# Optimization experiments

Measured on AMD Instinct MI355X. Metric: run time of the kernel, lower is better.

Reference implementation:

```python
import jax, jax.numpy as jnp
import numpy as np

L1, L2, L3 = 3072, 15, 32
NUM_PSQT = 8
NUM_LS = 8
NUM_FEATURES = 22528
B = 1024
MAX_ACTIVE = 32


def setup_inputs() -> dict:
    key = jax.random.key(0)
    ks = jax.random.split(key, 12)
    inp = {
        "us": jax.random.uniform(ks[0], (B, 1), dtype=jnp.float32),
        "them": jax.random.uniform(ks[1], (B, 1), dtype=jnp.float32),
        "white_indices": jax.random.randint(ks[2], (B, MAX_ACTIVE), 0, NUM_FEATURES, dtype=jnp.int64 if jax.config.jax_enable_x64 else jnp.int32),
        "white_values": jnp.ones((B, MAX_ACTIVE), dtype=jnp.float32),
        "black_indices": jax.random.randint(ks[3], (B, MAX_ACTIVE), 0, NUM_FEATURES, dtype=jnp.int64 if jax.config.jax_enable_x64 else jnp.int32),
        "black_values": jnp.ones((B, MAX_ACTIVE), dtype=jnp.float32),
        "psqt_indices": jax.random.randint(ks[4], (B,), 0, NUM_PSQT),
        "layer_stack_indices": jax.random.randint(ks[5], (B,), 0, NUM_LS),
        # feature transformer (sparse embedding) params: width L1 + NUM_PSQT
        "ft_weight": jax.random.normal(ks[6], (NUM_FEATURES, L1 + NUM_PSQT), dtype=jnp.float32) * 0.01,
        "ft_bias": jax.random.normal(ks[7], (L1 + NUM_PSQT,), dtype=jnp.float32) * 0.01,
        # bucketed layer stacks: l1 outputs L2 + 1 (extra unit is the skip connection)
        "W1": jax.random.normal(ks[8], (NUM_LS, L2 + 1, L1), dtype=jnp.float32) * 0.02,
        "b1": jnp.zeros((NUM_LS, L2 + 1), dtype=jnp.float32),
        "W2": jax.random.normal(ks[9], (NUM_LS, L3, 2 * L2), dtype=jnp.float32) * 0.1,
        "b2": jnp.zeros((NUM_LS, L3), dtype=jnp.float32),
        "W3": jax.random.normal(ks[10], (NUM_LS, 1, L3), dtype=jnp.float32) * 0.1,
        "b3": jnp.zeros((NUM_LS, 1), dtype=jnp.float32),
    }
    return inp


def _ft_accumulate(ft_weight, ft_bias, indices, values):
    # sparse feature accumulator: sum of gathered rows weighted by values
    rows = ft_weight[indices]                    # [B, F, L1+NUM_PSQT]
    return jnp.einsum("bfd,bf->bd", rows, values) + ft_bias


def _select_bucket(x_all, bucket_idx):
    # x_all: [B, K, D] -> [B, D] selecting per-sample bucket
    return jnp.take_along_axis(x_all, bucket_idx[:, None, None], axis=1)[:, 0]


def reference(us, them, white_indices, white_values, black_indices, black_values,
              psqt_indices, layer_stack_indices,
              ft_weight, ft_bias, W1, b1, W2, b2, W3, b3):
    wp = _ft_accumulate(ft_weight, ft_bias, white_indices, white_values)
    bp = _ft_accumulate(ft_weight, ft_bias, black_indices, black_values)
    w, wpsqt = wp[:, :L1], wp[:, L1:]
    b, bpsqt = bp[:, :L1], bp[:, L1:]

    # perspective mix + clamp + pairwise squared activation
    l0 = us * jnp.concatenate([w, b], axis=1) + them * jnp.concatenate([b, w], axis=1)
    l0 = jnp.clip(l0, 0.0, 1.0)                  # [B, 2*L1]
    h = L1 // 2
    l0 = jnp.concatenate([l0[:, :h] * l0[:, h:2 * h],
                          l0[:, 2 * h:3 * h] * l0[:, 3 * h:]], axis=1) * (127.0 / 128.0)  # [B, L1]

    # bucketed layer stacks (compute all buckets, tiny dims, then select)
    li = layer_stack_indices
    l1c = _select_bucket(jnp.einsum("bi,koi->bko", l0, W1) + b1, li)   # [B, L2+1]
    l1x, l1y = l1c[:, :L2], l1c[:, L2:]
    l1x = jnp.clip(jnp.concatenate([l1x * l1x, l1x], axis=1), 0.0, 1.0)  # [B, 2*L2]
    l2c = _select_bucket(jnp.einsum("bi,koi->bko", l1x, W2) + b2, li)  # [B, L3]
    l2x = jnp.clip(l2c, 0.0, 1.0)
    l3c = _select_bucket(jnp.einsum("bi,koi->bko", l2x, W3) + b3, li)  # [B, 1]
    ls_out = l3c + l1y

    # psqt gather + side-to-move sign
    wps = jnp.take_along_axis(wpsqt, psqt_indices[:, None], axis=1)    # [B, 1]
    bps = jnp.take_along_axis(bpsqt, psqt_indices[:, None], axis=1)
    return ls_out + (wps - bps) * (us - 0.5)
```

## Files before the change

### kernel.cpp

```cpp
#include <hip/hip_runtime.h>

__device__ __forceinline__ float clip01(float x) {
    return fminf(fmaxf(x, 0.0f), 1.0f);
}

__device__ __forceinline__ void fma4(float4& a, const float4 v, const float s) {
    a.x = fmaf(v.x, s, a.x);
    a.y = fmaf(v.y, s, a.y);
    a.z = fmaf(v.z, s, a.z);
    a.w = fmaf(v.w, s, a.w);
}

__device__ __forceinline__ float4 add4(const float4 a, const float4 b) {
    return make_float4(a.x + b.x, a.y + b.y, a.z + b.z, a.w + b.w);
}

__global__ __launch_bounds__(256) void nnue_fwd(
    const float* __restrict__ us_p,
    const float* __restrict__ them_p,
    const int*   __restrict__ wIdx,
    const float* __restrict__ wVal,
    const int*   __restrict__ bIdx,
    const float* __restrict__ bVal,
    const int*   __restrict__ psqtIdx,
    const int*   __restrict__ lsIdx,
    const float* __restrict__ ftw,
    const float* __restrict__ ftb,
    const float* __restrict__ W1,
    const float* __restrict__ b1,
    const float* __restrict__ W2,
    const float* __restrict__ b2,
    const float* __restrict__ W3,
    const float* __restrict__ b3,
    float* __restrict__ out)
{
    __shared__ __align__(16) float sw[3080];
    __shared__ __align__(16) float sb[3080];
    __shared__ __align__(16) float sl0[3072];
    __shared__ float sl1[16];

    const int b   = blockIdx.x;
    const int tid = threadIdx.x;

    float4 aw0 = {0,0,0,0}, aw1 = {0,0,0,0}, aw2 = {0,0,0,0}, awt = {0,0,0,0};
    float4 ab0 = {0,0,0,0}, ab1 = {0,0,0,0}, ab2 = {0,0,0,0}, abt = {0,0,0,0};

    const int*   wIp = wIdx + b * 32;
    const float* wVp = wVal + b * 32;
    const int*   bIp = bIdx + b * 32;
    const float* bVp = bVal + b * 32;

    for (int f = 0; f < 32; ++f) {
        const int   iw = wIp[f];
        const float vw = wVp[f];
        const int   ib = bIp[f];
        const float vb = bVp[f];
        const float4* rw = reinterpret_cast<const float4*>(ftw + (size_t)iw * 3080);
        const float4* rb = reinterpret_cast<const float4*>(ftw + (size_t)ib * 3080);

        float4 x0 = rw[tid];
        float4 x1 = rw[tid + 256];
        float4 x2 = rw[tid + 512];
        float4 y0 = rb[tid];
        float4 y1 = rb[tid + 256];
        float4 y2 = rb[tid + 512];
        fma4(aw0, x0, vw); fma4(aw1, x1, vw); fma4(aw2, x2, vw);
        fma4(ab0, y0, vb); fma4(ab1, y1, vb); fma4(ab2, y2, vb);
        if (tid < 2) {
            float4 xt = rw[768 + tid];
            float4 yt = rb[768 + tid];
            fma4(awt, xt, vw);
            fma4(abt, yt, vb);
        }
    }

    {
        const float4* bv  = reinterpret_cast<const float4*>(ftb);
        float4* swv = reinterpret_cast<float4*>(sw);
        float4* sbv = reinterpret_cast<float4*>(sb);
        float4 bb;
        bb = bv[tid];       swv[tid]       = add4(aw0, bb); sbv[tid]       = add4(ab0, bb);
        bb = bv[tid + 256]; swv[tid + 256] = add4(aw1, bb); sbv[tid + 256] = add4(ab1, bb);
        bb = bv[tid + 512]; swv[tid + 512] = add4(aw2, bb); sbv[tid + 512] = add4(ab2, bb);
        if (tid < 2) {
            bb = bv[768 + tid];
            swv[768 + tid] = add4(awt, bb);
            sbv[768 + tid] = add4(abt, bb);
        }
    }
    __syncthreads();

    const float u  = us_p[b];
    const float th = them_p[b];
    const float cmul = 127.0f / 128.0f;
    #pragma unroll
    for (int s = 0; s < 6; ++s) {
        const int j = tid + s * 256;
        const float w0 = sw[j],        w1 = sw[j + 1536];
        const float v0 = sb[j],        v1 = sb[j + 1536];
        const float a0 = clip01(u * w0 + th * v0);
        const float a1 = clip01(u * w1 + th * v1);
        const float c0 = clip01(u * v0 + th * w0);
        const float c1 = clip01(u * v1 + th * w1);
        sl0[j]        = a0 * a1 * cmul;
        sl0[1536 + j] = c0 * c1 * cmul;
    }
    __syncthreads();

    const int li = lsIdx[b];
    const float* W1b = W1 + (size_t)li * 16 * 3072;
    const int wave = tid >> 6;
    const int lane = tid & 63;
    const float4* l0v = reinterpret_cast<const float4*>(sl0);
    #pragma unroll
    for (int r0 = 0; r0 < 4; ++r0) {
        const int row = wave * 4 + r0;
        const float4* wr = reinterpret_cast<const float4*>(W1b + row * 3072);
        float acc = 0.0f;
        #pragma unroll
        for (int it = 0; it < 12; ++it) {
            const float4 a = wr[lane + it * 64];
            const float4 x = l0v[lane + it * 64];
            acc = fmaf(a.x, x.x, acc);
            acc = fmaf(a.y, x.y, acc);
            acc = fmaf(a.z, x.z, acc);
            acc = fmaf(a.w, x.w, acc);
        }
        #pragma unroll
        for (int off = 32; off > 0; off >>= 1) acc += __shfl_down(acc, off);
        if (lane == 0) sl1[row] = acc + b1[li * 16 + row];
    }
    __syncthreads();

    if (wave == 0) {
        float p = 0.0f;
        if (lane < 32) {
            const float* W2r = W2 + ((size_t)li * 32 + lane) * 30;
            float acc = b2[li * 32 + lane];
            #pragma unroll
            for (int i = 0; i < 30; ++i) {
                float v = (i < 15) ? sl1[i] * sl1[i] : sl1[i - 15];
                v = clip01(v);
                acc = fmaf(W2r[i], v, acc);
            }
            const float l2x = clip01(acc);
            p = l2x * W3[li * 32 + lane];
        }
        #pragma unroll
        for (int off = 32; off > 0; off >>= 1) p += __shfl_down(p, off);
        if (lane == 0) {
            const float l1y = sl1[15];
            const int   pi  = psqtIdx[b];
            const float wps = sw[3072 + pi];
            const float bps = sb[3072 + pi];
            out[b] = p + b3[li] + l1y + (wps - bps) * (u - 0.5f);
        }
    }
}

extern "C" void kernel_launch(void* const* d_in, const int* in_sizes, int n_in,
                              void* d_out, int out_size, void* d_ws, size_t ws_size,
                              hipStream_t stream) {
    const float* us_p   = (const float*)d_in[0];
    const float* them_p = (const float*)d_in[1];
    const int*   wIdx   = (const int*)d_in[2];
    const float* wVal   = (const float*)d_in[3];
    const int*   bIdx   = (const int*)d_in[4];
    const float* bVal   = (const float*)d_in[5];
    const int*   psqtI  = (const int*)d_in[6];
    const int*   lsI    = (const int*)d_in[7];
    const float* ftw    = (const float*)d_in[8];
    const float* ftb    = (const float*)d_in[9];
    const float* W1     = (const float*)d_in[10];
    const float* b1     = (const float*)d_in[11];
    const float* W2     = (const float*)d_in[12];
    const float* b2     = (const float*)d_in[13];
    const float* W3     = (const float*)d_in[14];
    const float* b3     = (const float*)d_in[15];
    float* out = (float*)d_out;

    const int B = in_sizes[0];
    nnue_fwd<<<B, 256, 0, stream>>>(us_p, them_p, wIdx, wVal, bIdx, bVal,
                                    psqtI, lsI, ftw, ftb, W1, b1, W2, b2, W3, b3, out);
}
```

Measured before the change: 128.7 us.

## Stage sparse indices in LDS, scalarize them, and unroll the gather by two

```diff
diff --git a/kernel.cpp b/kernel.cpp
--- a/kernel.cpp
+++ b/kernel.cpp
@@ -15,7 +15,14 @@
     return make_float4(a.x + b.x, a.y + b.y, a.z + b.z, a.w + b.w);
 }
 
-__global__ __launch_bounds__(256) void nnue_fwd(
+__device__ __forceinline__ int rdfl_i(int x) {
+    return __builtin_amdgcn_readfirstlane(x);
+}
+__device__ __forceinline__ float rdfl_f(float x) {
+    return __int_as_float(__builtin_amdgcn_readfirstlane(__float_as_int(x)));
+}
+
+__global__ __launch_bounds__(256, 4) void nnue_fwd(
     const float* __restrict__ us_p,
     const float* __restrict__ them_p,
     const int*   __restrict__ wIdx,
@@ -36,41 +43,55 @@
 {
     __shared__ __align__(16) float sw[3080];
     __shared__ __align__(16) float sb[3080];
-    __shared__ __align__(16) float sl0[3072];
     __shared__ float sl1[16];
+    __shared__ int   sIw[32], sIb[32];
+    __shared__ float sVw[32], sVb[32];
 
     const int b   = blockIdx.x;
     const int tid = threadIdx.x;
 
+    if (tid < 32) {
+        sIw[tid] = wIdx[b * 32 + tid];
+        sVw[tid] = wVal[b * 32 + tid];
+        sIb[tid] = bIdx[b * 32 + tid];
+        sVb[tid] = bVal[b * 32 + tid];
+    }
+    __syncthreads();
+
     float4 aw0 = {0,0,0,0}, aw1 = {0,0,0,0}, aw2 = {0,0,0,0}, awt = {0,0,0,0};
     float4 ab0 = {0,0,0,0}, ab1 = {0,0,0,0}, ab2 = {0,0,0,0}, abt = {0,0,0,0};
 
-    const int*   wIp = wIdx + b * 32;
-    const float* wVp = wVal + b * 32;
-    const int*   bIp = bIdx + b * 32;
-    const float* bVp = bVal + b * 32;
-
-    for (int f = 0; f < 32; ++f) {
-        const int   iw = wIp[f];
-        const float vw = wVp[f];
-        const int   ib = bIp[f];
-        const float vb = bVp[f];
-        const float4* rw = reinterpret_cast<const float4*>(ftw + (size_t)iw * 3080);
-        const float4* rb = reinterpret_cast<const float4*>(ftw + (size_t)ib * 3080);
-
-        float4 x0 = rw[tid];
-        float4 x1 = rw[tid + 256];
-        float4 x2 = rw[tid + 512];
-        float4 y0 = rb[tid];
-        float4 y1 = rb[tid + 256];
-        float4 y2 = rb[tid + 512];
-        fma4(aw0, x0, vw); fma4(aw1, x1, vw); fma4(aw2, x2, vw);
-        fma4(ab0, y0, vb); fma4(ab1, y1, vb); fma4(ab2, y2, vb);
+    #pragma unroll 1
+    for (int f = 0; f < 32; f += 2) {
+        const int   iw0 = rdfl_i(sIw[f]);
+        const int   ib0 = rdfl_i(sIb[f]);
+        const int   iw1 = rdfl_i(sIw[f + 1]);
+        const int   ib1 = rdfl_i(sIb[f + 1]);
+        const float vw0 = rdfl_f(sVw[f]);
+        const float vb0 = rdfl_f(sVb[f]);
+        const float vw1 = rdfl_f(sVw[f + 1]);
+        const float vb1 = rdfl_f(sVb[f + 1]);
+
+        const float4* rw0 = reinterpret_cast<const float4*>(ftw + (size_t)iw0 * 3080);
+        const float4* rb0 = reinterpret_cast<const float4*>(ftw + (size_t)ib0 * 3080);
+        const float4* rw1 = reinterpret_cast<const float4*>(ftw + (size_t)iw1 * 3080);
+        const float4* rb1 = reinterpret_cast<const float4*>(ftw + (size_t)ib1 * 3080);
+
+        const float4 xa0 = rw0[tid], xa1 = rw0[tid + 256], xa2 = rw0[tid + 512];
+        const float4 xb0 = rb0[tid], xb1 = rb0[tid + 256], xb2 = rb0[tid + 512];
+        const float4 xc0 = rw1[tid], xc1 = rw1[tid + 256], xc2 = rw1[tid + 512];
+        const float4 xd0 = rb1[tid], xd1 = rb1[tid + 256], xd2 = rb1[tid + 512];
+
+        fma4(aw0, xa0, vw0); fma4(aw1, xa1, vw0); fma4(aw2, xa2, vw0);
+        fma4(ab0, xb0, vb0); fma4(ab1, xb1, vb0); fma4(ab2, xb2, vb0);
+        fma4(aw0, xc0, vw1); fma4(aw1, xc1, vw1); fma4(aw2, xc2, vw1);
+        fma4(ab0, xd0, vb1); fma4(ab1, xd1, vb1); fma4(ab2, xd2, vb1);
+
         if (tid < 2) {
-            float4 xt = rw[768 + tid];
-            float4 yt = rb[768 + tid];
-            fma4(awt, xt, vw);
-            fma4(abt, yt, vb);
+            const float4 t0 = rw0[768 + tid], t1 = rb0[768 + tid];
+            const float4 t2 = rw1[768 + tid], t3 = rb1[768 + tid];
+            fma4(awt, t0, vw0); fma4(abt, t1, vb0);
+            fma4(awt, t2, vw1); fma4(abt, t3, vb1);
         }
     }
 
@@ -90,6 +111,7 @@
     }
     __syncthreads();
 
+    float* sl0 = sw;
     const float u  = us_p[b];
     const float th = them_p[b];
     const float cmul = 127.0f / 128.0f;
@@ -107,7 +129,7 @@
     }
     __syncthreads();
 
-    const int li = lsIdx[b];
+    const int li = rdfl_i(lsIdx[b]);
     const float* W1b = W1 + (size_t)li * 16 * 3072;
     const int wave = tid >> 6;
     const int lane = tid & 63;
```

Result: no change. 131.1 us (+1.9%).

## Convert feature-transformer weights to fp16 in workspace before gathering rows

Applied to the files above, without the earlier changes.

```diff
diff --git a/kernel.cpp b/kernel.cpp
--- a/kernel.cpp
+++ b/kernel.cpp
@@ -1,4 +1,9 @@
 #include <hip/hip_runtime.h>
+#include <hip/hip_fp16.h>
+
+#define FT_OUT 3080
+#define N_CHUNK 385
+#define N_ROWS 22528
 
 __device__ __forceinline__ float clip01(float x) {
     return fminf(fmaxf(x, 0.0f), 1.0f);
@@ -15,7 +20,174 @@
     return make_float4(a.x + b.x, a.y + b.y, a.z + b.z, a.w + b.w);
 }
 
-__global__ __launch_bounds__(256) void nnue_fwd(
+__device__ __forceinline__ void fma_h8(float* acc, const uint4 c, const float s) {
+    const __half2* h = reinterpret_cast<const __half2*>(&c);
+    #pragma unroll
+    for (int k = 0; k < 4; ++k) {
+        const float2 f = __half22float2(h[k]);
+        acc[2 * k]     = fmaf(f.x, s, acc[2 * k]);
+        acc[2 * k + 1] = fmaf(f.y, s, acc[2 * k + 1]);
+    }
+}
+
+__global__ __launch_bounds__(256) void convert_ftw(const float4* __restrict__ src,
+                                                   ushort4* __restrict__ dst, int n4) {
+    int i = blockIdx.x * 256 + threadIdx.x;
+    const int stride = gridDim.x * 256;
+    for (; i < n4; i += stride) {
+        const float4 v = src[i];
+        ushort4 h;
+        h.x = __half_as_ushort(__float2half_rn(v.x));
+        h.y = __half_as_ushort(__float2half_rn(v.y));
+        h.z = __half_as_ushort(__float2half_rn(v.z));
+        h.w = __half_as_ushort(__float2half_rn(v.w));
+        dst[i] = h;
+    }
+}
+
+__global__ __launch_bounds__(256, 4) void nnue_fwd_h(
+    const float* __restrict__ us_p,
+    const float* __restrict__ them_p,
+    const int*   __restrict__ wIdx,
+    const float* __restrict__ wVal,
+    const int*   __restrict__ bIdx,
+    const float* __restrict__ bVal,
+    const int*   __restrict__ psqtIdx,
+    const int*   __restrict__ lsIdx,
+    const __half* __restrict__ ftw_h,
+    const float* __restrict__ ftb,
+    const float* __restrict__ W1,
+    const float* __restrict__ b1,
+    const float* __restrict__ W2,
+    const float* __restrict__ b2,
+    const float* __restrict__ W3,
+    const float* __restrict__ b3,
+    float* __restrict__ out)
+{
+    __shared__ __align__(16) float sw[FT_OUT];
+    __shared__ __align__(16) float sb[FT_OUT];
+    __shared__ __align__(16) float sl0[3072];
+    __shared__ float sl1[16];
+
+    const int b   = blockIdx.x;
+    const int tid = threadIdx.x;
+
+    const int*   wIp = wIdx + b * 32;
+    const float* wVp = wVal + b * 32;
+    const int*   bIp = bIdx + b * 32;
+    const float* bVp = bVal + b * 32;
+
+    float accW0[8] = {0,0,0,0,0,0,0,0}, accW1[8] = {0,0,0,0,0,0,0,0};
+    float accB0[8] = {0,0,0,0,0,0,0,0}, accB1[8] = {0,0,0,0,0,0,0,0};
+    const bool tail = (tid < (N_CHUNK - 256));
+
+    for (int f = 0; f < 32; ++f) {
+        const int   iw = wIp[f];
+        const float vw = wVp[f];
+        const int   ib = bIp[f];
+        const float vb = bVp[f];
+        const uint4* rw = reinterpret_cast<const uint4*>(ftw_h + (size_t)iw * FT_OUT);
+        const uint4* rb = reinterpret_cast<const uint4*>(ftw_h + (size_t)ib * FT_OUT);
+
+        const uint4 cw0 = rw[tid];
+        const uint4 cb0 = rb[tid];
+        uint4 cw1, cb1;
+        if (tail) { cw1 = rw[256 + tid]; cb1 = rb[256 + tid]; }
+
+        fma_h8(accW0, cw0, vw);
+        fma_h8(accB0, cb0, vb);
+        if (tail) { fma_h8(accW1, cw1, vw); fma_h8(accB1, cb1, vb); }
+    }
+
+    {
+        const float4* bv  = reinterpret_cast<const float4*>(ftb);
+        float4* swv = reinterpret_cast<float4*>(sw);
+        float4* sbv = reinterpret_cast<float4*>(sb);
+        const float4 b0 = bv[2 * tid], b1v = bv[2 * tid + 1];
+        swv[2 * tid]     = make_float4(accW0[0] + b0.x, accW0[1] + b0.y, accW0[2] + b0.z, accW0[3] + b0.w);
+        swv[2 * tid + 1] = make_float4(accW0[4] + b1v.x, accW0[5] + b1v.y, accW0[6] + b1v.z, accW0[7] + b1v.w);
+        sbv[2 * tid]     = make_float4(accB0[0] + b0.x, accB0[1] + b0.y, accB0[2] + b0.z, accB0[3] + b0.w);
+        sbv[2 * tid + 1] = make_float4(accB0[4] + b1v.x, accB0[5] + b1v.y, accB0[6] + b1v.z, accB0[7] + b1v.w);
+        if (tail) {
+            const int c = 256 + tid;
+            const float4 b2v = bv[2 * c], b3v = bv[2 * c + 1];
+            swv[2 * c]     = make_float4(accW1[0] + b2v.x, accW1[1] + b2v.y, accW1[2] + b2v.z, accW1[3] + b2v.w);
+            swv[2 * c + 1] = make_float4(accW1[4] + b3v.x, accW1[5] + b3v.y, accW1[6] + b3v.z, accW1[7] + b3v.w);
+            sbv[2 * c]     = make_float4(accB1[0] + b2v.x, accB1[1] + b2v.y, accB1[2] + b2v.z, accB1[3] + b2v.w);
+            sbv[2 * c + 1] = make_float4(accB1[4] + b3v.x, accB1[5] + b3v.y, accB1[6] + b3v.z, accB1[7] + b3v.w);
+        }
+    }
+    __syncthreads();
+
+    const float u  = us_p[b];
+    const float th = them_p[b];
+    const float cmul = 127.0f / 128.0f;
+    #pragma unroll
+    for (int s = 0; s < 6; ++s) {
+        const int j = tid + s * 256;
+        const float w0 = sw[j],        w1 = sw[j + 1536];
+        const float v0 = sb[j],        v1 = sb[j + 1536];
+        const float a0 = clip01(u * w0 + th * v0);
+        const float a1 = clip01(u * w1 + th * v1);
+        const float c0 = clip01(u * v0 + th * w0);
+        const float c1 = clip01(u * v1 + th * w1);
+        sl0[j]        = a0 * a1 * cmul;
+        sl0[1536 + j] = c0 * c1 * cmul;
+    }
+    __syncthreads();
+
+    const int li = lsIdx[b];
+    const float* W1b = W1 + (size_t)li * 16 * 3072;
+    const int wave = tid >> 6;
+    const int lane = tid & 63;
+    const float4* l0v = reinterpret_cast<const float4*>(sl0);
+    #pragma unroll
+    for (int r0 = 0; r0 < 4; ++r0) {
+        const int row = wave * 4 + r0;
+        const float4* wr = reinterpret_cast<const float4*>(W1b + row * 3072);
+        float acc = 0.0f;
+        #pragma unroll
+        for (int it = 0; it < 12; ++it) {
+            const float4 a = wr[lane + it * 64];
+            const float4 x = l0v[lane + it * 64];
+            acc = fmaf(a.x, x.x, acc);
+            acc = fmaf(a.y, x.y, acc);
+            acc = fmaf(a.z, x.z, acc);
+            acc = fmaf(a.w, x.w, acc);
+        }
+        #pragma unroll
+        for (int off = 32; off > 0; off >>= 1) acc += __shfl_down(acc, off);
+        if (lane == 0) sl1[row] = acc + b1[li * 16 + row];
+    }
+    __syncthreads();
+
+    if (wave == 0) {
+        float p = 0.0f;
+        if (lane < 32) {
+            const float* W2r = W2 + ((size_t)li * 32 + lane) * 30;
+            float acc = b2[li * 32 + lane];
+            #pragma unroll
+            for (int i = 0; i < 30; ++i) {
+                float v = (i < 15) ? sl1[i] * sl1[i] : sl1[i - 15];
+                v = clip01(v);
+                acc = fmaf(W2r[i], v, acc);
+            }
+            const float l2x = clip01(acc);
+            p = l2x * W3[li * 32 + lane];
+        }
+        #pragma unroll
+        for (int off = 32; off > 0; off >>= 1) p += __shfl_down(p, off);
+        if (lane == 0) {
+            const float l1y = sl1[15];
+            const int   pi  = psqtIdx[b];
+            const float wps = sw[3072 + pi];
+            const float bps = sb[3072 + pi];
+            out[b] = p + b3[li] + l1y + (wps - bps) * (u - 0.5f);
+        }
+    }
+}
+
+__global__ __launch_bounds__(256) void nnue_fwd_f32(
     const float* __restrict__ us_p,
     const float* __restrict__ them_p,
     const int*   __restrict__ wIdx,
@@ -34,8 +206,8 @@
     const float* __restrict__ b3,
     float* __restrict__ out)
 {
-    __shared__ __align__(16) float sw[3080];
-    __shared__ __align__(16) float sb[3080];
+    __shared__ __align__(16) float sw[FT_OUT];
+    __shared__ __align__(16) float sb[FT_OUT];
     __shared__ __align__(16) float sl0[3072];
     __shared__ float sl1[16];
 
@@ -55,25 +227,18 @@
         const float vw = wVp[f];
         const int   ib = bIp[f];
         const float vb = bVp[f];
-        const float4* rw = reinterpret_cast<const float4*>(ftw + (size_t)iw * 3080);
-        const float4* rb = reinterpret_cast<const float4*>(ftw + (size_t)ib * 3080);
-
-        float4 x0 = rw[tid];
-        float4 x1 = rw[tid + 256];
-        float4 x2 = rw[tid + 512];
-        float4 y0 = rb[tid];
-        float4 y1 = rb[tid + 256];
-        float4 y2 = rb[tid + 512];
+        const float4* rw = reinterpret_cast<const float4*>(ftw + (size_t)iw * FT_OUT);
+        const float4* rb = reinterpret_cast<const float4*>(ftw + (size_t)ib * FT_OUT);
+
+        float4 x0 = rw[tid], x1 = rw[tid + 256], x2 = rw[tid + 512];
+        float4 y0 = rb[tid], y1 = rb[tid + 256], y2 = rb[tid + 512];
         fma4(aw0, x0, vw); fma4(aw1, x1, vw); fma4(aw2, x2, vw);
         fma4(ab0, y0, vb); fma4(ab1, y1, vb); fma4(ab2, y2, vb);
         if (tid < 2) {
-            float4 xt = rw[768 + tid];
-            float4 yt = rb[768 + tid];
-            fma4(awt, xt, vw);
-            fma4(abt, yt, vb);
-        }
-    }
-
+            float4 xt = rw[768 + tid], yt = rb[768 + tid];
+            fma4(awt, xt, vw); fma4(abt, yt, vb);
+        }
+    }
     {
         const float4* bv  = reinterpret_cast<const float4*>(ftb);
         float4* swv = reinterpret_cast<float4*>(sw);
@@ -151,9 +316,7 @@
         if (lane == 0) {
             const float l1y = sl1[15];
             const int   pi  = psqtIdx[b];
-            const float wps = sw[3072 + pi];
-            const float bps = sb[3072 + pi];
-            out[b] = p + b3[li] + l1y + (wps - bps) * (u - 0.5f);
+            out[b] = p + b3[li] + l1y + (sw[3072 + pi] - sb[3072 + pi]) * (u - 0.5f);
         }
     }
 }
@@ -180,6 +343,17 @@
     float* out = (float*)d_out;
 
     const int B = in_sizes[0];
-    nnue_fwd<<<B, 256, 0, stream>>>(us_p, them_p, wIdx, wVal, bIdx, bVal,
-                                    psqtI, lsI, ftw, ftb, W1, b1, W2, b2, W3, b3, out);
-}
+    const size_t need = (size_t)N_ROWS * FT_OUT * sizeof(__half);
+
+    if (ws_size >= need) {
+        __half* ftw_h = (__half*)d_ws;
+        const int n4 = N_ROWS * FT_OUT / 4;
+        convert_ftw<<<2048, 256, 0, stream>>>(
+            (const float4*)ftw, (ushort4*)ftw_h, n4);
+        nnue_fwd_h<<<B, 256, 0, stream>>>(us_p, them_p, wIdx, wVal, bIdx, bVal,
+                                          psqtI, lsI, ftw_h, ftb, W1, b1, W2, b2, W3, b3, out);
+    } else {
+        nnue_fwd_f32<<<B, 256, 0, stream>>>(us_p, them_p, wIdx, wVal, bIdx, bVal,
+                                            psqtI, lsI, ftw, ftb, W1, b1, W2, b2, W3, b3, out);
+    }
+}
```

New measurement: 139.8 us. +8.6%, slower.
